# Kernel tuning notes

Measured on AMD Instinct MI355X. Metric: run time of the kernel, lower is better.

## Reference

```python
import jax, jax.numpy as jnp
import numpy as np

NEG_SLOPE = 0.2  # LeakyReLU slope used by standard GAT


def setup_inputs() -> dict:
    key = jax.random.key(0)
    k1, k2, k3, k4, k5, k6 = jax.random.split(key, 6)
    N, E, F_in, F_out = 100000, 1600000, 256, 128
    x = jax.random.normal(k1, (N, F_in), dtype=jnp.float32)
    edge_index = jax.random.randint(k2, (2, E), 0, N, dtype=jnp.int32)
    W = jax.random.normal(k3, (F_in, F_out), dtype=jnp.float32) * (1.0 / np.sqrt(F_in))
    a_src = jax.random.normal(k4, (F_out,), dtype=jnp.float32) * 0.1
    a_dst = jax.random.normal(k5, (F_out,), dtype=jnp.float32) * 0.1
    return {"x": x, "edge_index": edge_index, "W": W, "a_src": a_src, "a_dst": a_dst}


def reference(x, edge_index, W, a_src, a_dst):
    N = x.shape[0]
    src, dst = edge_index[0], edge_index[1]

    Wh = x @ W                               # [N, F_out]
    alpha_src = Wh @ a_src                   # [N]
    alpha_dst = Wh @ a_dst                   # [N]

    e = alpha_src[src] + alpha_dst[dst]      # [E] raw edge scores
    e = jnp.where(e > 0, e, NEG_SLOPE * e)   # LeakyReLU(0.2)

    # segment softmax over incoming edges of each destination node
    seg_max = jax.ops.segment_max(e, dst, num_segments=N)          # [N]
    seg_max = jnp.where(jnp.isfinite(seg_max), seg_max, 0.0)
    e_exp = jnp.exp(e - seg_max[dst])                               # [E]
    denom = jax.ops.segment_sum(e_exp, dst, num_segments=N)         # [N]
    alpha = e_exp / (denom[dst] + 1e-16)                            # [E]

    # weighted aggregation of source messages
    msgs = alpha[:, None] * Wh[src]                                  # [E, F_out]
    out = jax.ops.segment_sum(msgs, dst, num_segments=N)             # [N, F_out]
    return jax.nn.elu(out)
```

## Files before the change

### kernel.cpp

```cpp
#include <hip/hip_runtime.h>
#include <math.h>

#define NEG_SLOPE 0.2f
#define BINSH 8
#define BCAP 6144

typedef __attribute__((ext_vector_type(8))) short bf16x8;
typedef __attribute__((ext_vector_type(4))) float f32x4;
typedef __attribute__((ext_vector_type(8))) unsigned short us8;

__device__ inline unsigned short f2b(float f) {
  union { float f; unsigned u; } v; v.f = f;
  unsigned r = v.u + 0x7fffu + ((v.u >> 16) & 1u);
  return (unsigned short)(r >> 16);
}

__device__ inline void gload_lds16(const void* g, void* l) {
  __builtin_amdgcn_global_load_lds(
      (const __attribute__((address_space(1))) void*)g,
      (__attribute__((address_space(3))) void*)l, 16, 0, 0);
}

__launch_bounds__(256)
__global__ void k_work1(const float* __restrict__ W, unsigned short* __restrict__ WtBs,
                        const int* __restrict__ src, const int* __restrict__ dst,
                        int* __restrict__ cursor, unsigned* __restrict__ binned,
                        int E, int NBUK) {
  int bid = blockIdx.x;
  int t = threadIdx.x;
  if (bid < 128) {
    int i = bid * 256 + t;
    int k = i >> 7, n = i & 127;
    int c = k >> 3, e = k & 7;
    WtBs[n * 256 + ((c ^ (n & 31)) << 3) + e] = f2b(W[(size_t)k * 128 + n]);
    return;
  }
  __shared__ int lh[512];
  for (int c = t; c < NBUK; c += 256) lh[c] = 0;
  __syncthreads();
  int base = (bid - 128) * 2048;
  int bq[8], rq[8]; unsigned pq[8];
#pragma unroll
  for (int q = 0; q < 8; ++q) {
    int j = base + q * 256 + t;
    if (j < E) {
      int d = dst[j], s = src[j];
      bq[q] = d >> BINSH;
      pq[q] = ((unsigned)s << 8) | (unsigned)(d & 255);
      rq[q] = atomicAdd(&lh[bq[q]], 1);
    } else bq[q] = -1;
  }
  __syncthreads();
  for (int c = t; c < NBUK; c += 256) { int cnt = lh[c]; if (cnt) lh[c] = atomicAdd(&cursor[c], cnt); }
  __syncthreads();
#pragma unroll
  for (int q = 0; q < 8; ++q)
    if (bq[q] >= 0) binned[(size_t)bq[q] * BCAP + lh[bq[q]] + rq[q]] = pq[q];
}

__launch_bounds__(512, 4)
__global__ void k_work2(const float* __restrict__ x, const unsigned short* __restrict__ WtBs,
                        const float* __restrict__ a_src, const float* __restrict__ a_dst,
                        unsigned short* __restrict__ WhB, float* __restrict__ asrc,
                        float* __restrict__ adst, int N, int nGemm,
                        const unsigned* __restrict__ binned, const int* __restrict__ cursor,
                        int* __restrict__ offsets, int* __restrict__ degs,
                        int* __restrict__ csr) {
  __shared__ __align__(16) unsigned char sbuf[65536];
  int t = threadIdx.x;
  if ((int)blockIdx.x < nGemm) {
    unsigned short* Bs = (unsigned short*)sbuf;
    unsigned short* Cs = (unsigned short*)sbuf;
    int lane = t & 63, wid = t >> 6;
    int lr = lane & 15, lh2 = lane >> 4;
    int m0 = blockIdx.x * 128;

#pragma unroll
    for (int i = 0; i < 8; ++i) {
      int chunk = i * 512 + t;
      gload_lds16((const char*)WtBs + (size_t)chunk * 16, (char*)sbuf + (size_t)chunk * 16);
    }

    int row = m0 + wid * 16 + lr;
    int rc = row < N ? row : N - 1;
    const float* xp = x + (size_t)rc * 256 + lh2 * 8;

    f32x4 acc[8];
#pragma unroll
    for (int f = 0; f < 8; ++f) acc[f] = (f32x4){0.f, 0.f, 0.f, 0.f};

    __syncthreads();

#pragma unroll
    for (int ks = 0; ks < 8; ++ks) {
      float4 u0 = *(const float4*)(xp + ks * 32);
      float4 u1 = *(const float4*)(xp + ks * 32 + 4);
      bf16x8 a;
      a[0] = (short)f2b(u0.x); a[1] = (short)f2b(u0.y);
      a[2] = (short)f2b(u0.z); a[3] = (short)f2b(u0.w);
      a[4] = (short)f2b(u1.x); a[5] = (short)f2b(u1.y);
      a[6] = (short)f2b(u1.z); a[7] = (short)f2b(u1.w);
#pragma unroll
      for (int f = 0; f < 8; ++f) {
        int n = lr + 16 * f;
        bf16x8 b = *(const bf16x8*)(Bs + n * 256 + (((ks * 4 + lh2) ^ (n & 31)) << 3));
        acc[f] = __builtin_amdgcn_mfma_f32_16x16x32_bf16(a, b, acc[f], 0, 0, 0);
      }
    }

    float asv[8], adv[8];
#pragma unroll
    for (int f = 0; f < 8; ++f) { asv[f] = a_src[lr + 16 * f]; adv[f] = a_dst[lr + 16 * f]; }
    float as_p[4] = {}, ad_p[4] = {};
#pragma unroll
    for (int f = 0; f < 8; ++f)
#pragma unroll
      for (int r = 0; r < 4; ++r) {
        as_p[r] += acc[f][r] * asv[f];
        ad_p[r] += acc[f][r] * adv[f];
      }
#pragma unroll
    for (int off = 1; off < 16; off <<= 1)
#pragma unroll
      for (int r = 0; r < 4; ++r) {
        as_p[r] += __shfl_xor(as_p[r], off);
        ad_p[r] += __shfl_xor(ad_p[r], off);
      }
    if (lr == 0) {
#pragma unroll
      for (int r = 0; r < 4; ++r) {
        int m = m0 + wid * 16 + lh2 * 4 + r;
        if (m < N) { asrc[m] = as_p[r]; adst[m] = ad_p[r]; }
      }
    }

    __syncthreads();
#pragma unroll
    for (int f = 0; f < 8; ++f)
#pragma unroll
      for (int r = 0; r < 4; ++r)
        Cs[(wid * 16 + lh2 * 4 + r) * 136 + lr + 16 * f] = f2b(acc[f][r]);
    __syncthreads();
#pragma unroll
    for (int i = 0; i < 4; ++i) {
      int chunk = i * 512 + t;
      int rw = chunk >> 4, c8 = chunk & 15;
      int m = m0 + rw;
      if (m < N)
        *(us8*)(WhB + (size_t)m * 128 + c8 * 8) = *(const us8*)(Cs + rw * 136 + c8 * 8);
    }
    return;
  }

  {
    int b = blockIdx.x - nGemm;
    int beg = b * BCAP, end = beg + cursor[b];
    int node0 = b << BINSH;
    int nn = N - node0; if (nn > 256) nn = 256; if (nn < 0) nn = 0;
    int* ldeg = (int*)sbuf;
    int* lcur = ldeg + 256;
    int* wp = lcur + 256;
    if (t < 256) ldeg[t] = 0;
    __syncthreads();
    for (int j = beg + t; j < end; j += 512) atomicAdd(&ldeg[binned[j] & 255u], 1);
    __syncthreads();
    if (t < 256) {
      int lane = t & 63, wid = t >> 6;
      int v = (t < nn) ? ldeg[t] : 0;
      int incl = v;
#pragma unroll
      for (int off = 1; off < 64; off <<= 1) { int u = __shfl_up(incl, off); if (lane >= off) incl += u; }
      if (lane == 63) wp[wid] = incl;
      lcur[t] = incl - v;
    }
    __syncthreads();
    if (t < 256) {
      int wid = t >> 6;
      int add = 0;
      for (int k = 0; k < wid; ++k) add += wp[k];
      int ex = add + lcur[t];
      int v = (t < nn) ? ldeg[t] : 0;
      if (t < nn) { offsets[node0 + t] = beg + ex; degs[node0 + t] = v; }
      lcur[t] = ex;
    }
    __syncthreads();
    for (int j = beg + t; j < end; j += 512) {
      unsigned e = binned[j];
      int r = atomicAdd(&lcur[e & 255u], 1);
      csr[beg + r] = (int)(e >> 8);
    }
  }
}

__launch_bounds__(256)
__global__ void k_agg(const int* __restrict__ csr, const int* __restrict__ offsets,
                      const int* __restrict__ degs,
                      const unsigned short* __restrict__ WhB, const float* __restrict__ asrc,
                      const float* __restrict__ adst, float* __restrict__ out, int N) {
  int gt = blockIdx.x * blockDim.x + threadIdx.x;
  int wave = gt >> 6;
  int lane = gt & 63;
  int lq = lane & 15;
  int g = lane >> 4;
  int node = wave * 4 + g;
  if (node >= N) return;
  int beg = offsets[node];
  int end = beg + degs[node];
  float ad = adst[node];
  float acc[8] = {};
  float psum = 0.f;
  for (int chunk = beg; chunk < end; chunk += 16) {
    int j = chunk + lq;
    float p = 0.f; int mys = 0;
    if (j < end) {
      mys = csr[j];
      float e = asrc[mys] + ad;
      e = e > 0.f ? e : NEG_SLOPE * e;
      p = __expf(e);
    }
    psum += p;
#pragma unroll
    for (int tt = 0; tt < 8; ++tt) {
      float pt = __shfl(p, tt, 16);
      int st = __shfl(mys, tt, 16);
      uint4 v = *(const uint4*)(WhB + (size_t)(unsigned)st * 128u + lq * 8);
      acc[0] = fmaf(pt, __uint_as_float(v.x << 16), acc[0]);
      acc[1] = fmaf(pt, __uint_as_float(v.x & 0xffff0000u), acc[1]);
      acc[2] = fmaf(pt, __uint_as_float(v.y << 16), acc[2]);
      acc[3] = fmaf(pt, __uint_as_float(v.y & 0xffff0000u), acc[3]);
      acc[4] = fmaf(pt, __uint_as_float(v.z << 16), acc[4]);
      acc[5] = fmaf(pt, __uint_as_float(v.z & 0xffff0000u), acc[5]);
      acc[6] = fmaf(pt, __uint_as_float(v.w << 16), acc[6]);
      acc[7] = fmaf(pt, __uint_as_float(v.w & 0xffff0000u), acc[7]);
    }
    __builtin_amdgcn_sched_barrier(0);
#pragma unroll
    for (int tt = 8; tt < 16; ++tt) {
      float pt = __shfl(p, tt, 16);
      int st = __shfl(mys, tt, 16);
      uint4 v = *(const uint4*)(WhB + (size_t)(unsigned)st * 128u + lq * 8);
      acc[0] = fmaf(pt, __uint_as_float(v.x << 16), acc[0]);
      acc[1] = fmaf(pt, __uint_as_float(v.x & 0xffff0000u), acc[1]);
      acc[2] = fmaf(pt, __uint_as_float(v.y << 16), acc[2]);
      acc[3] = fmaf(pt, __uint_as_float(v.y & 0xffff0000u), acc[3]);
      acc[4] = fmaf(pt, __uint_as_float(v.z << 16), acc[4]);
      acc[5] = fmaf(pt, __uint_as_float(v.z & 0xffff0000u), acc[5]);
      acc[6] = fmaf(pt, __uint_as_float(v.w << 16), acc[6]);
      acc[7] = fmaf(pt, __uint_as_float(v.w & 0xffff0000u), acc[7]);
    }
  }
  psum += __shfl_xor(psum, 1);
  psum += __shfl_xor(psum, 2);
  psum += __shfl_xor(psum, 4);
  psum += __shfl_xor(psum, 8);
  float inv = 1.f / (psum + 1e-16f);
  size_t obase = (size_t)node * 128 + lq * 8;
  float r[8];
#pragma unroll
  for (int i = 0; i < 8; ++i) {
    float o = acc[i] * inv;
    r[i] = o > 0.f ? o : __expf(o) - 1.f;
  }
  f32x4 lo = {r[0], r[1], r[2], r[3]};
  f32x4 hi = {r[4], r[5], r[6], r[7]};
  __builtin_nontemporal_store(lo, (f32x4*)(out + obase));
  __builtin_nontemporal_store(hi, (f32x4*)(out + obase + 4));
}

extern "C" void kernel_launch(void* const* d_in, const int* in_sizes, int n_in,
                              void* d_out, int out_size, void* d_ws, size_t ws_size,
                              hipStream_t stream) {
  const float* x = (const float*)d_in[0];
  const int* ei = (const int*)d_in[1];
  const float* W = (const float*)d_in[2];
  const float* a_src = (const float*)d_in[3];
  const float* a_dst = (const float*)d_in[4];
  int N = in_sizes[0] / 256;
  int E = in_sizes[1] / 2;
  const int* src = ei;
  const int* dst = ei + E;
  float* out = (float*)d_out;
  int NBUK = (N + 255) >> BINSH;
  size_t REG = (size_t)NBUK * BCAP;

  unsigned short* WhB = (unsigned short*)d_ws;
  unsigned* binned = (unsigned*)(WhB + (size_t)N * 128);
  int* csr = (int*)(binned + REG);
  float* asrc = (float*)(csr + REG);
  float* adst = asrc + N;
  unsigned short* WtBs = (unsigned short*)(adst + N);
  int* cursor = (int*)(WtBs + 32768);
  int* offsets = cursor + NBUK;
  int* degs = offsets + N;

  int nBinA = (E + 2047) / 2048;
  int nGemm = (N + 127) / 128;

  hipMemsetAsync(cursor, 0, (size_t)NBUK * sizeof(int), stream);
  k_work1<<<128 + nBinA, 256, 0, stream>>>(W, WtBs, src, dst, cursor, binned, E, NBUK);
  k_work2<<<nGemm + NBUK, 512, 0, stream>>>(x, WtBs, a_src, a_dst, WhB, asrc, adst, N, nGemm,
                                            binned, cursor, offsets, degs, csr);
  k_agg<<<(N + 15) / 16, 256, 0, stream>>>(csr, offsets, degs, WhB, asrc, adst, out, N);
}
```

Before: 138.3 us.

## Stage x tiles through swizzled LDS via async loads, store Wh directly

The GEMM branch now loads each 32-column slice of x into a new XOR-swizzled LDS region with global_load_lds before converting it to bf16 for MFMA. Previously each lane read its rows straight from global memory. The change also removes the LDS staging of the bf16 output and writes Wh with scattered 2-byte global stores. The shared buffer grows from 64KB to 80KB, which may cut occupancy, and the loop adds two barriers per k-step with no double buffering.

```diff
diff --git a/kernel.cpp b/kernel.cpp
--- a/kernel.cpp
+++ b/kernel.cpp
@@ -66,11 +66,11 @@
                         const unsigned* __restrict__ binned, const int* __restrict__ cursor,
                         int* __restrict__ offsets, int* __restrict__ degs,
                         int* __restrict__ csr) {
-  __shared__ __align__(16) unsigned char sbuf[65536];
+  __shared__ __align__(16) unsigned char sbuf[81920];
   int t = threadIdx.x;
   if ((int)blockIdx.x < nGemm) {
     unsigned short* Bs = (unsigned short*)sbuf;
-    unsigned short* Cs = (unsigned short*)sbuf;
+    float* As = (float*)(sbuf + 65536);
     int lane = t & 63, wid = t >> 6;
     int lr = lane & 15, lh2 = lane >> 4;
     int m0 = blockIdx.x * 128;
@@ -81,31 +81,38 @@
       gload_lds16((const char*)WtBs + (size_t)chunk * 16, (char*)sbuf + (size_t)chunk * 16);
     }
 
-    int row = m0 + wid * 16 + lr;
-    int rc = row < N ? row : N - 1;
-    const float* xp = x + (size_t)rc * 256 + lh2 * 8;
-
+    int rowr = wid * 16 + lr;
+    int rs = rowr & 7;
     f32x4 acc[8];
 #pragma unroll
     for (int f = 0; f < 8; ++f) acc[f] = (f32x4){0.f, 0.f, 0.f, 0.f};
 
-    __syncthreads();
-
-#pragma unroll
-    for (int ks = 0; ks < 8; ++ks) {
-      float4 u0 = *(const float4*)(xp + ks * 32);
-      float4 u1 = *(const float4*)(xp + ks * 32 + 4);
+    for (int s = 0; s < 8; ++s) {
+#pragma unroll
+      for (int i = 0; i < 2; ++i) {
+        int chunk = i * 512 + t;
+        int row = chunk >> 3, c = chunk & 7;
+        int m = m0 + row; if (m >= N) m = N - 1;
+        int cs = c ^ (row & 7);
+        gload_lds16(x + (size_t)m * 256 + s * 32 + cs * 4, (char*)As + (size_t)chunk * 16);
+      }
+      __syncthreads();
+
+      int j0 = lh2 * 2;
+      f32x4 u0 = *(const f32x4*)(As + rowr * 32 + ((j0 ^ rs) << 2));
+      f32x4 u1 = *(const f32x4*)(As + rowr * 32 + (((j0 + 1) ^ rs) << 2));
       bf16x8 a;
-      a[0] = (short)f2b(u0.x); a[1] = (short)f2b(u0.y);
-      a[2] = (short)f2b(u0.z); a[3] = (short)f2b(u0.w);
-      a[4] = (short)f2b(u1.x); a[5] = (short)f2b(u1.y);
-      a[6] = (short)f2b(u1.z); a[7] = (short)f2b(u1.w);
+      a[0] = (short)f2b(u0[0]); a[1] = (short)f2b(u0[1]);
+      a[2] = (short)f2b(u0[2]); a[3] = (short)f2b(u0[3]);
+      a[4] = (short)f2b(u1[0]); a[5] = (short)f2b(u1[1]);
+      a[6] = (short)f2b(u1[2]); a[7] = (short)f2b(u1[3]);
 #pragma unroll
       for (int f = 0; f < 8; ++f) {
         int n = lr + 16 * f;
-        bf16x8 b = *(const bf16x8*)(Bs + n * 256 + (((ks * 4 + lh2) ^ (n & 31)) << 3));
+        bf16x8 b = *(const bf16x8*)(Bs + n * 256 + (((s * 4 + lh2) ^ (n & 31)) << 3));
         acc[f] = __builtin_amdgcn_mfma_f32_16x16x32_bf16(a, b, acc[f], 0, 0, 0);
       }
+      __syncthreads();
     }
 
     float asv[8], adv[8];
@@ -134,20 +141,14 @@
       }
     }
 
-    __syncthreads();
-#pragma unroll
-    for (int f = 0; f < 8; ++f)
-#pragma unroll
-      for (int r = 0; r < 4; ++r)
-        Cs[(wid * 16 + lh2 * 4 + r) * 136 + lr + 16 * f] = f2b(acc[f][r]);
-    __syncthreads();
-#pragma unroll
-    for (int i = 0; i < 4; ++i) {
-      int chunk = i * 512 + t;
-      int rw = chunk >> 4, c8 = chunk & 15;
-      int m = m0 + rw;
-      if (m < N)
-        *(us8*)(WhB + (size_t)m * 128 + c8 * 8) = *(const us8*)(Cs + rw * 136 + c8 * 8);
+#pragma unroll
+    for (int r = 0; r < 4; ++r) {
+      int m = m0 + wid * 16 + lh2 * 4 + r;
+      if (m < N) {
+#pragma unroll
+        for (int f = 0; f < 8; ++f)
+          WhB[(size_t)m * 128 + lr + 16 * f] = f2b(acc[f][r]);
+      }
     }
     return;
   }
```

New measurement: 139.7 us. No clear change (+1.0%).

## Double-buffer x tiles into LDS with async global loads in GEMM stage

Applied to the files above, without the earlier changes.

The GEMM branch of k_work2 now stages x row tiles into a swizzled double-buffered LDS region with global_load_lds, overlapping the load of the next K slice with MFMA compute on the current one, instead of each lane reading x directly from global memory. LDS grows from 64 KB to 128 KB and the occupancy hint drops from 4 to 2 blocks. This aims to hide global-load latency and improve coalescing, at the cost of fewer resident blocks and explicit barriers and waitcnt sequencing.

```diff
diff --git a/kernel.cpp b/kernel.cpp
--- a/kernel.cpp
+++ b/kernel.cpp
@@ -58,7 +58,7 @@
     if (bq[q] >= 0) binned[(size_t)bq[q] * BCAP + lh[bq[q]] + rq[q]] = pq[q];
 }
 
-__launch_bounds__(512, 4)
+__launch_bounds__(512, 2)
 __global__ void k_work2(const float* __restrict__ x, const unsigned short* __restrict__ WtBs,
                         const float* __restrict__ a_src, const float* __restrict__ a_dst,
                         unsigned short* __restrict__ WhB, float* __restrict__ asrc,
@@ -66,7 +66,7 @@
                         const unsigned* __restrict__ binned, const int* __restrict__ cursor,
                         int* __restrict__ offsets, int* __restrict__ degs,
                         int* __restrict__ csr) {
-  __shared__ __align__(16) unsigned char sbuf[65536];
+  __shared__ __align__(16) unsigned char sbuf[131072];
   int t = threadIdx.x;
   if ((int)blockIdx.x < nGemm) {
     unsigned short* Bs = (unsigned short*)sbuf;
@@ -74,39 +74,85 @@
     int lane = t & 63, wid = t >> 6;
     int lr = lane & 15, lh2 = lane >> 4;
     int m0 = blockIdx.x * 128;
+    int rowr = wid * 16 + lr;
+    int rsw = rowr & 15;
+
+    auto stageA = [&](int s, int buf) {
+#pragma unroll
+      for (int i = 0; i < 4; ++i) {
+        int chunk = i * 512 + t;
+        int row = chunk >> 4, c = chunk & 15;
+        int m = m0 + row; if (m >= N) m = N - 1;
+        int cs = c ^ (row & 15);
+        gload_lds16(x + (size_t)m * 256 + s * 64 + cs * 4,
+                    (char*)sbuf + 65536 + buf * 32768 + (size_t)chunk * 16);
+      }
+    };
+
+    f32x4 acc[8];
+#pragma unroll
+    for (int f = 0; f < 8; ++f) acc[f] = (f32x4){0.f, 0.f, 0.f, 0.f};
+
+    auto compute = [&](int s, int buf) {
+      const float* Ab = (const float*)(sbuf + 65536 + buf * 32768);
+#pragma unroll
+      for (int ks2 = 0; ks2 < 2; ++ks2) {
+        int j0 = ks2 * 8 + lh2 * 2;
+        f32x4 u0 = *(const f32x4*)(Ab + rowr * 64 + ((j0 ^ rsw) << 2));
+        f32x4 u1 = *(const f32x4*)(Ab + rowr * 64 + (((j0 + 1) ^ rsw) << 2));
+        bf16x8 a;
+        a[0] = (short)f2b(u0[0]); a[1] = (short)f2b(u0[1]);
+        a[2] = (short)f2b(u0[2]); a[3] = (short)f2b(u0[3]);
+        a[4] = (short)f2b(u1[0]); a[5] = (short)f2b(u1[1]);
+        a[6] = (short)f2b(u1[2]); a[7] = (short)f2b(u1[3]);
+#pragma unroll
+        for (int f = 0; f < 8; ++f) {
+          int n = lr + 16 * f;
+          bf16x8 b = *(const bf16x8*)(Bs + n * 256 +
+                                      (((s * 8 + ks2 * 4 + lh2) ^ (n & 31)) << 3));
+          acc[f] = __builtin_amdgcn_mfma_f32_16x16x32_bf16(a, b, acc[f], 0, 0, 0);
+        }
+      }
+    };
 
 #pragma unroll
     for (int i = 0; i < 8; ++i) {
       int chunk = i * 512 + t;
       gload_lds16((const char*)WtBs + (size_t)chunk * 16, (char*)sbuf + (size_t)chunk * 16);
     }
-
-    int row = m0 + wid * 16 + lr;
-    int rc = row < N ? row : N - 1;
-    const float* xp = x + (size_t)rc * 256 + lh2 * 8;
-
-    f32x4 acc[8];
-#pragma unroll
-    for (int f = 0; f < 8; ++f) acc[f] = (f32x4){0.f, 0.f, 0.f, 0.f};
-
-    __syncthreads();
-
-#pragma unroll
-    for (int ks = 0; ks < 8; ++ks) {
-      float4 u0 = *(const float4*)(xp + ks * 32);
-      float4 u1 = *(const float4*)(xp + ks * 32 + 4);
-      bf16x8 a;
-      a[0] = (short)f2b(u0.x); a[1] = (short)f2b(u0.y);
-      a[2] = (short)f2b(u0.z); a[3] = (short)f2b(u0.w);
-      a[4] = (short)f2b(u1.x); a[5] = (short)f2b(u1.y);
-      a[6] = (short)f2b(u1.z); a[7] = (short)f2b(u1.w);
-#pragma unroll
-      for (int f = 0; f < 8; ++f) {
-        int n = lr + 16 * f;
-        bf16x8 b = *(const bf16x8*)(Bs + n * 256 + (((ks * 4 + lh2) ^ (n & 31)) << 3));
-        acc[f] = __builtin_amdgcn_mfma_f32_16x16x32_bf16(a, b, acc[f], 0, 0, 0);
-      }
-    }
+    stageA(0, 0);
+    stageA(1, 1);
+    __builtin_amdgcn_sched_barrier(0);
+    asm volatile("s_waitcnt vmcnt(4)" ::: "memory");
+    __builtin_amdgcn_s_barrier();
+    __builtin_amdgcn_sched_barrier(0);
+
+    compute(0, 0);
+    __builtin_amdgcn_sched_barrier(0);
+    __builtin_amdgcn_s_barrier();
+    stageA(2, 0);
+    __builtin_amdgcn_sched_barrier(0);
+    asm volatile("s_waitcnt vmcnt(4)" ::: "memory");
+    __builtin_amdgcn_s_barrier();
+    __builtin_amdgcn_sched_barrier(0);
+
+    compute(1, 1);
+    __builtin_amdgcn_sched_barrier(0);
+    __builtin_amdgcn_s_barrier();
+    stageA(3, 1);
+    __builtin_amdgcn_sched_barrier(0);
+    asm volatile("s_waitcnt vmcnt(4)" ::: "memory");
+    __builtin_amdgcn_s_barrier();
+    __builtin_amdgcn_sched_barrier(0);
+
+    compute(2, 0);
+    __builtin_amdgcn_sched_barrier(0);
+    __builtin_amdgcn_s_barrier();
+    asm volatile("s_waitcnt vmcnt(0)" ::: "memory");
+    __builtin_amdgcn_s_barrier();
+    __builtin_amdgcn_sched_barrier(0);
+
+    compute(3, 1);
 
     float asv[8], adv[8];
 #pragma unroll
```

New measurement: 145.3 us. 5.0% more time.
